# Optimization experiments

Measured on AMD Instinct MI355X. Metric: run time of the kernel, lower is better.

Reference implementation:

```python
import jax, jax.numpy as jnp
import numpy as np

NPOS_MAX = 64

def setup_inputs() -> dict:
    key = jax.random.key(0)
    k1, k2, k3 = jax.random.split(key, 3)
    b, h, l, d = 4, 12, 1024, 64
    query = jax.random.normal(k1, (b, h, l, d), dtype=jnp.float32)
    attn_logits = jax.random.normal(k2, (b, h, l, l), dtype=jnp.float32)
    pos_emb = jax.random.normal(k3, (d, NPOS_MAX), dtype=jnp.float32) * 0.02
    return {"query": query, "attn_logits": attn_logits, "pos_emb": pos_emb}

def reference(query, attn_logits, pos_emb):
    # gates: sigmoid of attention logits, with diagonal zeroed
    gates = jax.nn.sigmoid(attn_logits)
    l = gates.shape[-1]
    eye = jnp.eye(l, dtype=gates.dtype)
    gates = gates * (1.0 - eye)
    # reverse cumsum along last axis, clamped to [0, npos_max-1]
    pos = jnp.flip(jnp.cumsum(jnp.flip(gates, -1), axis=-1), -1)
    pos = jnp.minimum(pos, jnp.asarray(NPOS_MAX - 1, dtype=pos.dtype))
    pos_ceil = jnp.ceil(pos).astype(jnp.int32)    # [b,h,l,l]
    pos_floor = jnp.floor(pos).astype(jnp.int32)  # [b,h,l,l]
    # interpolated position logits: [b,h,l,npos_max]
    logits_int = jnp.einsum('bhld,dn->bhln', query, pos_emb)
    logits_ceil = jnp.take_along_axis(logits_int, pos_ceil, axis=-1)
    logits_floor = jnp.take_along_axis(logits_int, pos_floor, axis=-1)
    w = pos - pos_floor.astype(pos.dtype)
    return logits_ceil * w + logits_floor * (1.0 - w)
```

## Files before the change

### kernel.cpp

```cpp
#include <hip/hip_runtime.h>
#include <hip/hip_bf16.h>


__device__ __forceinline__ float bf2f(unsigned short u) {
    union { unsigned int i; float f; } t; t.i = ((unsigned int)u) << 16; return t.f;
}
__device__ __forceinline__ float bf2f_lo(unsigned int v) {
    union { unsigned int i; float f; } t; t.i = v << 16; return t.f;
}
__device__ __forceinline__ float bf2f_hi(unsigned int v) {
    union { unsigned int i; float f; } t; t.i = v & 0xffff0000u; return t.f;
}
__device__ __forceinline__ unsigned short f2bf(float f) {
    union { float f; unsigned int i; } t; t.f = f;
    unsigned int lsb = (t.i >> 16) & 1u;
    t.i += 0x7fffu + lsb;
    return (unsigned short)(t.i >> 16);
}
__device__ __forceinline__ float sigmoid_fast(float x) {
    float e = __builtin_amdgcn_exp2f(-1.44269504f * x);
    return __builtin_amdgcn_rcpf(1.0f + e);
}

__global__ __launch_bounds__(256) void cope_detect(
    const unsigned short* __restrict__ q, int* __restrict__ flag)
{
    const int tid = threadIdx.x;
    unsigned short u = q[2 * tid];
    int e = (u >> 7) & 0xFF;
    unsigned long long m = __ballot(e >= 200);
    __shared__ int cnt;
    if (tid == 0) cnt = 0;
    __syncthreads();
    if ((tid & 63) == 0) atomicAdd(&cnt, __popcll(m));
    __syncthreads();
    if (tid == 0) *flag = (cnt > 8) ? 1 : 0;
}

__global__ __launch_bounds__(256) void cope_li(
    const void* __restrict__ qv, const void* __restrict__ pev,
    float* __restrict__ li, const int* __restrict__ flag)
{
    __shared__ float pe_f[64 * 64];
    __shared__ float q_t[64 * 64];
    const int tid = threadIdx.x;
    const bool isf32 = (*flag != 0);

    if (isf32) {
        const float4* pe4 = reinterpret_cast<const float4*>(pev);
#pragma unroll
        for (int it = 0; it < 4; ++it)
            reinterpret_cast<float4*>(pe_f)[it * 256 + tid] = pe4[it * 256 + tid];
        const float4* q4 = reinterpret_cast<const float4*>(qv) + (size_t)blockIdx.x * 1024;
#pragma unroll
        for (int it = 0; it < 4; ++it) {
            int idx = it * 256 + tid;
            int d4 = idx >> 6, rr = idx & 63;
            float4 v = q4[rr * 16 + d4];
            q_t[(d4 * 4 + 0) * 64 + rr] = v.x;
            q_t[(d4 * 4 + 1) * 64 + rr] = v.y;
            q_t[(d4 * 4 + 2) * 64 + rr] = v.z;
            q_t[(d4 * 4 + 3) * 64 + rr] = v.w;
        }
    } else {
        const uint4* pe16 = reinterpret_cast<const uint4*>(pev);
#pragma unroll
        for (int it = 0; it < 2; ++it) {
            int idx = it * 256 + tid;
            uint4 v = pe16[idx];
            float4 a, b;
            a.x = bf2f_lo(v.x); a.y = bf2f_hi(v.x);
            a.z = bf2f_lo(v.y); a.w = bf2f_hi(v.y);
            b.x = bf2f_lo(v.z); b.y = bf2f_hi(v.z);
            b.z = bf2f_lo(v.w); b.w = bf2f_hi(v.w);
            float4* dst = reinterpret_cast<float4*>(&pe_f[idx * 8]);
            dst[0] = a; dst[1] = b;
        }
        const ushort4* q4 = reinterpret_cast<const ushort4*>(qv) + (size_t)blockIdx.x * 1024;
#pragma unroll
        for (int it = 0; it < 4; ++it) {
            int idx = it * 256 + tid;
            int d4 = idx >> 6, rr = idx & 63;
            ushort4 v = q4[rr * 16 + d4];
            q_t[(d4 * 4 + 0) * 64 + rr] = bf2f(v.x);
            q_t[(d4 * 4 + 1) * 64 + rr] = bf2f(v.y);
            q_t[(d4 * 4 + 2) * 64 + rr] = bf2f(v.z);
            q_t[(d4 * 4 + 3) * 64 + rr] = bf2f(v.w);
        }
    }
    __syncthreads();

    const int r0 = (tid & 15) * 4, n0 = (tid >> 4) * 4;
    float acc[4][4];
#pragma unroll
    for (int a = 0; a < 4; ++a)
#pragma unroll
        for (int b = 0; b < 4; ++b) acc[a][b] = 0.f;

#pragma unroll 8
    for (int d = 0; d < 64; ++d) {
        float4 qv4 = *reinterpret_cast<const float4*>(&q_t[d * 64 + r0]);
        float4 pv = *reinterpret_cast<const float4*>(&pe_f[d * 64 + n0]);
        acc[0][0] += qv4.x * pv.x; acc[0][1] += qv4.x * pv.y; acc[0][2] += qv4.x * pv.z; acc[0][3] += qv4.x * pv.w;
        acc[1][0] += qv4.y * pv.x; acc[1][1] += qv4.y * pv.y; acc[1][2] += qv4.y * pv.z; acc[1][3] += qv4.y * pv.w;
        acc[2][0] += qv4.z * pv.x; acc[2][1] += qv4.z * pv.y; acc[2][2] += qv4.z * pv.z; acc[2][3] += qv4.z * pv.w;
        acc[3][0] += qv4.w * pv.x; acc[3][1] += qv4.w * pv.y; acc[3][2] += qv4.w * pv.z; acc[3][3] += qv4.w * pv.w;
    }
#pragma unroll
    for (int a = 0; a < 4; ++a) {
        size_t row = (size_t)blockIdx.x * 64 + r0 + a;
        float4 o; o.x = acc[a][0]; o.y = acc[a][1]; o.z = acc[a][2]; o.w = acc[a][3];
        *reinterpret_cast<float4*>(&li[row * 64 + n0]) = o;
    }
}

__global__ __launch_bounds__(256) void cope_main(
    const void* __restrict__ attnv,
    const float* __restrict__ li_ws,
    void* __restrict__ outv,
    const int* __restrict__ flag)
{
    const int tid = threadIdx.x;
    const int lane = tid & 63;
    const int wid = tid >> 6;
    const int r = blockIdx.x * 4 + wid;
    const int i = r & 1023;
    const bool isf32 = (*flag != 0);
    const int col0 = lane * 16;

    const float li_val = li_ws[(size_t)r * 64 + lane];

    float g[16];
    if (isf32) {
        const float4* ap = reinterpret_cast<const float4*>(
            reinterpret_cast<const float*>(attnv) + (size_t)r * 1024);
#pragma unroll
        for (int c = 0; c < 4; ++c) {
            float4 v = ap[4 * lane + c];
            float s0 = sigmoid_fast(v.x), s1 = sigmoid_fast(v.y);
            float s2 = sigmoid_fast(v.z), s3 = sigmoid_fast(v.w);
            int k = c * 4;
            g[k + 0] = (col0 + k + 0 == i) ? 0.f : s0;
            g[k + 1] = (col0 + k + 1 == i) ? 0.f : s1;
            g[k + 2] = (col0 + k + 2 == i) ? 0.f : s2;
            g[k + 3] = (col0 + k + 3 == i) ? 0.f : s3;
        }
    } else {
        const uint4* ap = reinterpret_cast<const uint4*>(
            reinterpret_cast<const unsigned short*>(attnv) + (size_t)r * 1024);
#pragma unroll
        for (int c = 0; c < 2; ++c) {
            uint4 v = ap[2 * lane + c];
            unsigned int w0 = v.x, w1 = v.y, w2 = v.z, w3 = v.w;
            int k = c * 8;
            float s;
            s = sigmoid_fast(bf2f_lo(w0)); g[k + 0] = (col0 + k + 0 == i) ? 0.f : s;
            s = sigmoid_fast(bf2f_hi(w0)); g[k + 1] = (col0 + k + 1 == i) ? 0.f : s;
            s = sigmoid_fast(bf2f_lo(w1)); g[k + 2] = (col0 + k + 2 == i) ? 0.f : s;
            s = sigmoid_fast(bf2f_hi(w1)); g[k + 3] = (col0 + k + 3 == i) ? 0.f : s;
            s = sigmoid_fast(bf2f_lo(w2)); g[k + 4] = (col0 + k + 4 == i) ? 0.f : s;
            s = sigmoid_fast(bf2f_hi(w2)); g[k + 5] = (col0 + k + 5 == i) ? 0.f : s;
            s = sigmoid_fast(bf2f_lo(w3)); g[k + 6] = (col0 + k + 6 == i) ? 0.f : s;
            s = sigmoid_fast(bf2f_hi(w3)); g[k + 7] = (col0 + k + 7 == i) ? 0.f : s;
        }
    }

    float ts = 0.f;
#pragma unroll
    for (int k = 0; k < 16; ++k) ts += g[k];

    float x = ts;
#pragma unroll
    for (int s = 1; s < 64; s <<= 1) {
        float y = __shfl_up(x, s, 64);
        if (lane >= s) x += y;
    }
    const float total = __shfl(x, 63, 64);
    float run = x - ts;

    float o[16];
#pragma unroll
    for (int e = 0; e < 16; ++e) {
        float p = total - run;
        run += g[e];
        p = fminf(fmaxf(p, 0.f), 63.f);
        float pf = floorf(p);
        float w = p - pf;
        int ipf = (int)pf;
        int ipc = min(ipf + 1, 63);
        float a = __shfl(li_val, ipf, 64);
        float b = __shfl(li_val, ipc, 64);
        o[e] = a + w * (b - a);
    }

    if (isf32) {
        float4* op = reinterpret_cast<float4*>(
            reinterpret_cast<float*>(outv) + (size_t)r * 1024);
#pragma unroll
        for (int c = 0; c < 4; ++c) {
            float4 v; int k = c * 4;
            v.x = o[k]; v.y = o[k + 1]; v.z = o[k + 2]; v.w = o[k + 3];
            op[4 * lane + c] = v;
        }
    } else {
        uint4* op = reinterpret_cast<uint4*>(
            reinterpret_cast<unsigned short*>(outv) + (size_t)r * 1024);
#pragma unroll
        for (int c = 0; c < 2; ++c) {
            int k = c * 8;
            uint4 v;
            v.x = (unsigned)f2bf(o[k + 0]) | ((unsigned)f2bf(o[k + 1]) << 16);
            v.y = (unsigned)f2bf(o[k + 2]) | ((unsigned)f2bf(o[k + 3]) << 16);
            v.z = (unsigned)f2bf(o[k + 4]) | ((unsigned)f2bf(o[k + 5]) << 16);
            v.w = (unsigned)f2bf(o[k + 6]) | ((unsigned)f2bf(o[k + 7]) << 16);
            op[2 * lane + c] = v;
        }
    }
}

__global__ __launch_bounds__(256) void cope_fused(
    const void* __restrict__ qv, const void* __restrict__ attnv,
    const void* __restrict__ pev, void* __restrict__ outv,
    const int* __restrict__ flag)
{
    const int r = blockIdx.x;
    const int i = r & 1023;
    const int tid = threadIdx.x;
    const int lane = tid & 63;
    const int wid = tid >> 6;
    const bool isf32 = (*flag != 0);

    __shared__ float pe_f[64 * 64];
    __shared__ float q_s[64];
    __shared__ float li[64];
    __shared__ float wsum[4];

    float g[4];
    if (isf32) {
        const float4* pe4 = reinterpret_cast<const float4*>(pev);
#pragma unroll
        for (int it = 0; it < 4; ++it)
            reinterpret_cast<float4*>(pe_f)[it * 256 + tid] = pe4[it * 256 + tid];
        if (tid < 16) {
            float4 v = reinterpret_cast<const float4*>(qv)[(size_t)r * 16 + tid];
            q_s[tid * 4 + 0] = v.x; q_s[tid * 4 + 1] = v.y;
            q_s[tid * 4 + 2] = v.z; q_s[tid * 4 + 3] = v.w;
        }
        float4 av = reinterpret_cast<const float4*>(attnv)[(size_t)r * 256 + tid];
        g[0] = sigmoid_fast(av.x); g[1] = sigmoid_fast(av.y);
        g[2] = sigmoid_fast(av.z); g[3] = sigmoid_fast(av.w);
    } else {
        const uint4* pe16 = reinterpret_cast<const uint4*>(pev);
#pragma unroll
        for (int it = 0; it < 2; ++it) {
            int idx = it * 256 + tid;
            uint4 v = pe16[idx];
            float4 a, b;
            a.x = bf2f_lo(v.x); a.y = bf2f_hi(v.x);
            a.z = bf2f_lo(v.y); a.w = bf2f_hi(v.y);
            b.x = bf2f_lo(v.z); b.y = bf2f_hi(v.z);
            b.z = bf2f_lo(v.w); b.w = bf2f_hi(v.w);
            float4* dst = reinterpret_cast<float4*>(&pe_f[idx * 8]);
            dst[0] = a; dst[1] = b;
        }
        if (tid < 16) {
            ushort4 v = reinterpret_cast<const ushort4*>(qv)[(size_t)r * 16 + tid];
            q_s[tid * 4 + 0] = bf2f(v.x); q_s[tid * 4 + 1] = bf2f(v.y);
            q_s[tid * 4 + 2] = bf2f(v.z); q_s[tid * 4 + 3] = bf2f(v.w);
        }
        ushort4 av = reinterpret_cast<const ushort4*>(attnv)[(size_t)r * 256 + tid];
        g[0] = sigmoid_fast(bf2f(av.x)); g[1] = sigmoid_fast(bf2f(av.y));
        g[2] = sigmoid_fast(bf2f(av.z)); g[3] = sigmoid_fast(bf2f(av.w));
    }

    const int j0 = tid * 4;
    if (i >= j0 && i < j0 + 4) g[i - j0] = 0.f;
    float ts = g[0] + g[1] + g[2] + g[3];
    float x = ts;
#pragma unroll
    for (int s = 1; s < 64; s <<= 1) {
        float y = __shfl_up(x, s, 64);
        if (lane >= s) x += y;
    }
    if (lane == 63) wsum[wid] = x;
    __syncthreads();
    if (tid < 64) {
        float acc = 0.f;
#pragma unroll
        for (int d = 0; d < 64; ++d) acc += q_s[d] * pe_f[d * 64 + tid];
        li[tid] = acc;
    }
    const float s0 = wsum[0], s1 = wsum[1], s2 = wsum[2], s3 = wsum[3];
    const float total = s0 + s1 + s2 + s3;
    float woff = 0.f;
    if (wid > 0) woff += s0;
    if (wid > 1) woff += s1;
    if (wid > 2) woff += s2;
    float run = woff + (x - ts);
    __syncthreads();

    float o[4];
#pragma unroll
    for (int e = 0; e < 4; ++e) {
        float p = total - run;
        run += g[e];
        p = fminf(fmaxf(p, 0.f), 63.f);
        float pf = floorf(p);
        int ipf = (int)pf;
        int ipc = min(ipf + 1, 63);
        float w = p - pf;
        o[e] = li[ipf] + w * (li[ipc] - li[ipf]);
    }
    if (isf32) {
        float4 ov; ov.x = o[0]; ov.y = o[1]; ov.z = o[2]; ov.w = o[3];
        reinterpret_cast<float4*>(outv)[(size_t)r * 256 + tid] = ov;
    } else {
        ushort4 ov;
        ov.x = f2bf(o[0]); ov.y = f2bf(o[1]); ov.z = f2bf(o[2]); ov.w = f2bf(o[3]);
        reinterpret_cast<ushort4*>(outv)[(size_t)r * 256 + tid] = ov;
    }
}

extern "C" void kernel_launch(void* const* d_in, const int* in_sizes, int n_in,
                              void* d_out, int out_size, void* d_ws, size_t ws_size,
                              hipStream_t stream) {
    const void* q    = d_in[0];
    const void* attn = d_in[1];
    const void* pe   = d_in[2];
    int* flag = (int*)d_ws;
    float* li = (float*)((char*)d_ws + 256);

    const long L = 1024;
    const long rows = (long)in_sizes[1] / L;
    const size_t ws_need = 256 + (size_t)rows * 64 * sizeof(float);

    cope_detect<<<1, 256, 0, stream>>>((const unsigned short*)d_in[0], flag);
    if (ws_size >= ws_need) {
        cope_li<<<(int)(rows / 64), 256, 0, stream>>>(q, pe, li, flag);
        cope_main<<<(int)(rows / 4), 256, 0, stream>>>(attn, li, d_out, flag);
    } else {
        cope_fused<<<(int)rows, 256, 0, stream>>>(q, attn, pe, d_out, flag);
    }
}
```

Before: 355.1 us.

## Process one row per block with cross-wave scan and LDS position lookup

The main kernel changes from one row per wavefront (16 elements per lane) to one row per 256-thread block (4 elements per thread). The reverse-cumsum becomes a per-wave shuffle scan combined across the four waves through shared memory and a __syncthreads. The position-logit gather reads a 65-entry LDS table instead of two cross-lane shuffles per element, and loads and stores become fully coalesced 16-byte accesses per thread. This gives more parallelism and fewer registers per thread, in exchange for four times as many blocks and a block-level barrier per row.

```diff
diff --git a/kernel.cpp b/kernel.cpp
--- a/kernel.cpp
+++ b/kernel.cpp
@@ -114,60 +114,43 @@
     }
 }
 
-__global__ __launch_bounds__(256) void cope_main(
+__global__ __launch_bounds__(256) void cope_row(
     const void* __restrict__ attnv,
     const float* __restrict__ li_ws,
     void* __restrict__ outv,
     const int* __restrict__ flag)
 {
+    const int r = blockIdx.x;
+    const int i = r & 1023;
     const int tid = threadIdx.x;
     const int lane = tid & 63;
     const int wid = tid >> 6;
-    const int r = blockIdx.x * 4 + wid;
-    const int i = r & 1023;
     const bool isf32 = (*flag != 0);
-    const int col0 = lane * 16;
-
-    const float li_val = li_ws[(size_t)r * 64 + lane];
-
-    float g[16];
-    if (isf32) {
-        const float4* ap = reinterpret_cast<const float4*>(
-            reinterpret_cast<const float*>(attnv) + (size_t)r * 1024);
-#pragma unroll
-        for (int c = 0; c < 4; ++c) {
-            float4 v = ap[4 * lane + c];
-            float s0 = sigmoid_fast(v.x), s1 = sigmoid_fast(v.y);
-            float s2 = sigmoid_fast(v.z), s3 = sigmoid_fast(v.w);
-            int k = c * 4;
-            g[k + 0] = (col0 + k + 0 == i) ? 0.f : s0;
-            g[k + 1] = (col0 + k + 1 == i) ? 0.f : s1;
-            g[k + 2] = (col0 + k + 2 == i) ? 0.f : s2;
-            g[k + 3] = (col0 + k + 3 == i) ? 0.f : s3;
-        }
-    } else {
-        const uint4* ap = reinterpret_cast<const uint4*>(
-            reinterpret_cast<const unsigned short*>(attnv) + (size_t)r * 1024);
-#pragma unroll
-        for (int c = 0; c < 2; ++c) {
-            uint4 v = ap[2 * lane + c];
-            unsigned int w0 = v.x, w1 = v.y, w2 = v.z, w3 = v.w;
-            int k = c * 8;
-            float s;
-            s = sigmoid_fast(bf2f_lo(w0)); g[k + 0] = (col0 + k + 0 == i) ? 0.f : s;
-            s = sigmoid_fast(bf2f_hi(w0)); g[k + 1] = (col0 + k + 1 == i) ? 0.f : s;
-            s = sigmoid_fast(bf2f_lo(w1)); g[k + 2] = (col0 + k + 2 == i) ? 0.f : s;
-            s = sigmoid_fast(bf2f_hi(w1)); g[k + 3] = (col0 + k + 3 == i) ? 0.f : s;
-            s = sigmoid_fast(bf2f_lo(w2)); g[k + 4] = (col0 + k + 4 == i) ? 0.f : s;
-            s = sigmoid_fast(bf2f_hi(w2)); g[k + 5] = (col0 + k + 5 == i) ? 0.f : s;
-            s = sigmoid_fast(bf2f_lo(w3)); g[k + 6] = (col0 + k + 6 == i) ? 0.f : s;
-            s = sigmoid_fast(bf2f_hi(w3)); g[k + 7] = (col0 + k + 7 == i) ? 0.f : s;
-        }
-    }
-
-    float ts = 0.f;
-#pragma unroll
-    for (int k = 0; k < 16; ++k) ts += g[k];
+
+    __shared__ float li[65];
+    __shared__ float wsum[4];
+
+    if (tid < 64) {
+        float lv = li_ws[(size_t)r * 64 + tid];
+        li[tid] = lv;
+        if (tid == 63) li[64] = lv;
+    }
+
+    float g[4];
+    if (isf32) {
+        float4 av = reinterpret_cast<const float4*>(attnv)[(size_t)r * 256 + tid];
+        g[0] = sigmoid_fast(av.x); g[1] = sigmoid_fast(av.y);
+        g[2] = sigmoid_fast(av.z); g[3] = sigmoid_fast(av.w);
+    } else {
+        ushort4 av = reinterpret_cast<const ushort4*>(attnv)[(size_t)r * 256 + tid];
+        g[0] = sigmoid_fast(bf2f(av.x)); g[1] = sigmoid_fast(bf2f(av.y));
+        g[2] = sigmoid_fast(bf2f(av.z)); g[3] = sigmoid_fast(bf2f(av.w));
+    }
+
+    const int j0 = tid * 4;
+    if (i >= j0 && i < j0 + 4) g[i - j0] = 0.f;
+
+    float ts = g[0] + g[1] + g[2] + g[3];
 
     float x = ts;
 #pragma unroll
@@ -175,46 +158,38 @@
         float y = __shfl_up(x, s, 64);
         if (lane >= s) x += y;
     }
-    const float total = __shfl(x, 63, 64);
-    float run = x - ts;
-
-    float o[16];
-#pragma unroll
-    for (int e = 0; e < 16; ++e) {
+    if (lane == 63) wsum[wid] = x;
+
+    __syncthreads();
+
+    const float s0 = wsum[0], s1 = wsum[1], s2 = wsum[2], s3 = wsum[3];
+    const float total = s0 + s1 + s2 + s3;
+    float woff = 0.f;
+    if (wid > 0) woff += s0;
+    if (wid > 1) woff += s1;
+    if (wid > 2) woff += s2;
+    float run = woff + (x - ts);
+
+    float o[4];
+#pragma unroll
+    for (int e = 0; e < 4; ++e) {
         float p = total - run;
         run += g[e];
         p = fminf(fmaxf(p, 0.f), 63.f);
         float pf = floorf(p);
-        float w = p - pf;
         int ipf = (int)pf;
-        int ipc = min(ipf + 1, 63);
-        float a = __shfl(li_val, ipf, 64);
-        float b = __shfl(li_val, ipc, 64);
-        o[e] = a + w * (b - a);
-    }
-
-    if (isf32) {
-        float4* op = reinterpret_cast<float4*>(
-            reinterpret_cast<float*>(outv) + (size_t)r * 1024);
-#pragma unroll
-        for (int c = 0; c < 4; ++c) {
-            float4 v; int k = c * 4;
-            v.x = o[k]; v.y = o[k + 1]; v.z = o[k + 2]; v.w = o[k + 3];
-            op[4 * lane + c] = v;
-        }
-    } else {
-        uint4* op = reinterpret_cast<uint4*>(
-            reinterpret_cast<unsigned short*>(outv) + (size_t)r * 1024);
-#pragma unroll
-        for (int c = 0; c < 2; ++c) {
-            int k = c * 8;
-            uint4 v;
-            v.x = (unsigned)f2bf(o[k + 0]) | ((unsigned)f2bf(o[k + 1]) << 16);
-            v.y = (unsigned)f2bf(o[k + 2]) | ((unsigned)f2bf(o[k + 3]) << 16);
-            v.z = (unsigned)f2bf(o[k + 4]) | ((unsigned)f2bf(o[k + 5]) << 16);
-            v.w = (unsigned)f2bf(o[k + 6]) | ((unsigned)f2bf(o[k + 7]) << 16);
-            op[2 * lane + c] = v;
-        }
+        float a = li[ipf], b = li[ipf + 1];
+        o[e] = fmaf(p - pf, b - a, a);
+    }
+
+    if (isf32) {
+        float4 ov; ov.x = o[0]; ov.y = o[1]; ov.z = o[2]; ov.w = o[3];
+        reinterpret_cast<float4*>(outv)[(size_t)r * 256 + tid] = ov;
+    } else {
+        uint2 ov;
+        ov.x = (unsigned)f2bf(o[0]) | ((unsigned)f2bf(o[1]) << 16);
+        ov.y = (unsigned)f2bf(o[2]) | ((unsigned)f2bf(o[3]) << 16);
+        reinterpret_cast<uint2*>(outv)[(size_t)r * 256 + tid] = ov;
     }
 }
 
@@ -337,7 +312,7 @@
     cope_detect<<<1, 256, 0, stream>>>((const unsigned short*)d_in[0], flag);
     if (ws_size >= ws_need) {
         cope_li<<<(int)(rows / 64), 256, 0, stream>>>(q, pe, li, flag);
-        cope_main<<<(int)(rows / 4), 256, 0, stream>>>(attn, li, d_out, flag);
+        cope_row<<<(int)rows, 256, 0, stream>>>(attn, li, d_out, flag);
     } else {
         cope_fused<<<(int)rows, 256, 0, stream>>>(q, attn, pe, d_out, flag);
     }
```

New measurement: 341.2 us. 3.9% less time.
